# Kernel tuning notes

Measured on AMD Instinct MI355X. Metric: run time of the kernel, lower is better.

## Reference

```python
import jax, jax.numpy as jnp
import numpy as np

N_GENES = 15135
N_CMT = 1000
HID = 64


def _gcn_norm(edge_index, n):
    # add self-loops, compute symmetric normalization deg^-1/2 * deg^-1/2
    loop = jnp.arange(n, dtype=edge_index.dtype)
    src = jnp.concatenate([edge_index[0], loop])
    dst = jnp.concatenate([edge_index[1], loop])
    deg = jax.ops.segment_sum(jnp.ones_like(src, dtype=jnp.float32), dst, num_segments=n)
    dinv = jnp.where(deg > 0, 1.0 / jnp.sqrt(deg), 0.0)
    return src, dst, dinv[src] * dinv[dst]


def _gcn_conv(x, W, b, src, dst, norm, n):
    h = x @ W                                  # [bs, N, H]
    m = h[:, src, :] * norm[None, :, None]     # gather messages [bs, E, H]
    out = jnp.zeros_like(h).at[:, dst, :].add(m)
    return out + b


def setup_inputs():
    key = jax.random.key(0)
    ks = jax.random.split(key, 16)
    bs, nf, hfc, ncls, E, P = 8, 64, 128, 2, 242160, 120000
    s = 0.05
    return {
        "x": jax.random.normal(ks[0], (bs, N_GENES, nf), jnp.float32),
        "batch": jnp.zeros((bs,), jnp.int32),
        "edge_index": jax.random.randint(ks[1], (2, E), 0, N_GENES),
        "path_row": jax.random.randint(ks[2], (P,), 0, N_GENES),
        "path_col": jax.random.randint(ks[3], (P,), 0, N_CMT),
        "W1": jax.random.normal(ks[4], (nf, HID), jnp.float32) * s,
        "b1": jnp.zeros((HID,), jnp.float32),
        "W2": jax.random.normal(ks[5], (HID, HID), jnp.float32) * s,
        "b2": jnp.zeros((HID,), jnp.float32),
        "W3": jax.random.normal(ks[6], (HID, HID), jnp.float32) * s,
        "b3": jnp.zeros((HID,), jnp.float32),
        "fcW": jax.random.normal(ks[7], (3 * HID, 1), jnp.float32) * s,
        "fcb": jnp.zeros((1,), jnp.float32),
        "l1W": jax.random.normal(ks[8], (N_CMT, hfc), jnp.float32) * s,
        "l1b": jnp.zeros((hfc,), jnp.float32),
        "l2W": jax.random.normal(ks[9], (hfc, ncls), jnp.float32) * s,
        "l2b": jnp.zeros((ncls,), jnp.float32),
    }


def reference(x, batch, edge_index, path_row, path_col,
              W1, b1, W2, b2, W3, b3, fcW, fcb, l1W, l1b, l2W, l2b):
    bs, n = x.shape[0], x.shape[1]
    src, dst, norm = _gcn_norm(edge_index, n)

    x1 = jax.nn.relu(_gcn_conv(x, W1, b1, src, dst, norm, n))
    x2 = jax.nn.relu(_gcn_conv(x1, W2, b2, src, dst, norm, n))
    x3 = jax.nn.relu(_gcn_conv(x2, W3, b3, src, dst, norm, n))
    # mode='cat': torch.stack(xs, -1).view(bs, N, -1) -> layout [..., h*L + l]
    xc = jnp.stack([x1, x2, x3], axis=-1).reshape(bs, n, HID * 3)

    # pathway pooling: scatter_mean(x[row], col) over node axis
    xt = jnp.transpose(xc, (1, 0, 2))            # [N, bs, F]
    g = xt[path_row]                             # [P, bs, F]
    sums = jax.ops.segment_sum(g, path_col, num_segments=N_CMT)
    cnt = jax.ops.segment_sum(jnp.ones_like(path_col, dtype=xc.dtype), path_col, num_segments=N_CMT)
    pooled = sums / jnp.maximum(cnt, 1.0)[:, None, None]   # [n_cmt, bs, F]
    pooled = jnp.transpose(pooled, (1, 0, 2)).reshape(-1, HID * 3)  # [bs*n_cmt, F]

    h = (pooled @ fcW + fcb).reshape(bs, N_CMT)   # fc -> view(-1, n_cmt)
    h = jax.nn.relu(h @ l1W + l1b)                # (dropout is identity in eval)
    h = h @ l2W + l2b
    return jax.nn.log_softmax(h, axis=-1)
```

## Files before the change

kernel.cpp:

```cpp
#include <hip/hip_runtime.h>
#include <hip/hip_bf16.h>
#include <hip/hip_fp16.h>
#include <math.h>

#define HID 64

#if defined(__has_builtin)
#if __has_builtin(__builtin_amdgcn_cvt_pk_f32_fp8) && __has_builtin(__builtin_amdgcn_cvt_pk_fp8_f32)
#define HWFP8 1
#endif
#endif

typedef float vfloat2 __attribute__((ext_vector_type(2)));
typedef __attribute__((ext_vector_type(8))) short short8_t;
typedef __attribute__((ext_vector_type(4))) float f32x4;

union ABFrag { short8_t s; unsigned short u[8]; };


__device__ __forceinline__ unsigned short f2bf(float x) {
    unsigned int u = __float_as_uint(x);
    unsigned int r = u + 0x7fffu + ((u >> 16) & 1u);
    return (unsigned short)(r >> 16);
}

#ifndef HWFP8
__device__ __forceinline__ unsigned int enc8_sw(float a) {
    unsigned short hb = __half_as_ushort(__float2half(a));
    unsigned int r = (unsigned int)hb + 0x7fu + ((hb >> 8) & 1u);
    return (r >> 8) & 0xffu;
}
__device__ __forceinline__ float dec8_sw(unsigned int b) {
    return __half2float(__ushort_as_half((unsigned short)(b << 8)));
}
#endif

__device__ __forceinline__ unsigned int enc4(float a, float b, float c, float d) {
#ifdef HWFP8
    int r = __builtin_amdgcn_cvt_pk_fp8_f32(a, b, 0, false);
    r = __builtin_amdgcn_cvt_pk_fp8_f32(c, d, r, true);
    return (unsigned int)r;
#else
    return enc8_sw(a) | (enc8_sw(b) << 8) | (enc8_sw(c) << 16) | (enc8_sw(d) << 24);
#endif
}

__device__ __forceinline__ void dec4(unsigned int w, float* f) {
#ifdef HWFP8
    vfloat2 a = __builtin_amdgcn_cvt_pk_f32_fp8((int)w, false);
    vfloat2 b = __builtin_amdgcn_cvt_pk_f32_fp8((int)w, true);
    f[0] = a.x; f[1] = a.y; f[2] = b.x; f[3] = b.y;
#else
    f[0] = dec8_sw(w & 0xffu); f[1] = dec8_sw((w >> 8) & 0xffu);
    f[2] = dec8_sw((w >> 16) & 0xffu); f[3] = dec8_sw(w >> 24);
#endif
}

__device__ __forceinline__ void dec8(uint2 g, float* f) {
    dec4(g.x, f);
    dec4(g.y, f + 4);
}

__device__ __forceinline__ void gemm_epilogue(float* so, const f32x4* acc,
                                              unsigned int* Yq, float S,
                                              int r0w, int rowsTot, int lane) {
    int cc = lane & 15;
    int cr = (lane >> 4) * 4;
#pragma unroll
    for (int c = 0; c < 4; ++c) {
        so[(cr + 0) * 68 + c * 16 + cc] = acc[c][0];
        so[(cr + 1) * 68 + c * 16 + cc] = acc[c][1];
        so[(cr + 2) * 68 + c * 16 + cc] = acc[c][2];
        so[(cr + 3) * 68 + c * 16 + cc] = acc[c][3];
    }
    __syncthreads();
#pragma unroll
    for (int i = 0; i < 4; ++i) {
        int idx = lane + i * 64;
        int row = idx >> 4, ci = idx & 15;
        int grow = r0w + row;
        if (grow < rowsTot) {
            float4 v = *(const float4*)&so[row * 68 + ci * 4];
            Yq[(size_t)grow * 16 + ci] = enc4(v.x * S, v.y * S, v.z * S, v.w * S);
        }
    }
}

__global__ __launch_bounds__(256) void k_fused1(const float* __restrict__ x,
                                                const float* __restrict__ W1,
                                                unsigned int* __restrict__ Yq,
                                                float S, int N, int rowsTot, int gGf,
                                                const int* __restrict__ edst, int* __restrict__ deg, int E,
                                                const int* __restrict__ pcol, int* __restrict__ ccnt, int P,
                                                const float* __restrict__ W2, const float* __restrict__ W3,
                                                unsigned short* __restrict__ Wt) {
    __shared__ float sOut[4][16 * 68];
    __shared__ unsigned short sW[4096];
    int tid = threadIdx.x;
    if ((int)blockIdx.x < gGf) {
        int w = tid >> 6, lane = tid & 63;
        int cc = lane & 15, kg = (lane >> 4) * 8;
        float* so = &sOut[w][0];
#pragma unroll
        for (int i = 0; i < 16; ++i) {
            int idx = i * 256 + tid;
            int k = idx >> 6, c = idx & 63;
            sW[c * 64 + k] = f2bf(W1[idx]);
        }
        __syncthreads();
        ABFrag bf[2][4];
#pragma unroll
        for (int h = 0; h < 2; ++h)
#pragma unroll
            for (int c = 0; c < 4; ++c)
                bf[h][c].s = *(const short8_t*)&sW[(c * 16 + cc) * 64 + h * 32 + kg];

        int base = blockIdx.x * 128;
        ABFrag a[2];
        auto loadA = [&](int rA, ABFrag* dst) {
#pragma unroll
            for (int h = 0; h < 2; ++h) {
                if (rA < rowsTot) {
                    int n = rA >> 3, b = rA & 7;
                    const float* p = &x[((size_t)b * N + n) * 64 + h * 32 + kg];
                    float4 v0 = *(const float4*)p;
                    float4 v1 = *(const float4*)(p + 4);
                    dst[h].u[0] = f2bf(v0.x); dst[h].u[1] = f2bf(v0.y);
                    dst[h].u[2] = f2bf(v0.z); dst[h].u[3] = f2bf(v0.w);
                    dst[h].u[4] = f2bf(v1.x); dst[h].u[5] = f2bf(v1.y);
                    dst[h].u[6] = f2bf(v1.z); dst[h].u[7] = f2bf(v1.w);
                } else {
#pragma unroll
                    for (int j = 0; j < 8; ++j) dst[h].u[j] = 0;
                }
            }
        };
        loadA(base + w * 16 + (lane & 15), a);
#pragma unroll
        for (int t = 0; t < 2; ++t) {
            ABFrag an[2];
            if (t < 1) loadA(base + 64 + w * 16 + (lane & 15), an);
            f32x4 acc[4] = {f32x4{}, f32x4{}, f32x4{}, f32x4{}};
#pragma unroll
            for (int h = 0; h < 2; ++h)
#pragma unroll
                for (int c = 0; c < 4; ++c)
                    acc[c] = __builtin_amdgcn_mfma_f32_16x16x32_bf16(a[h].s, bf[h][c].s, acc[c], 0, 0, 0);
            gemm_epilogue(so, acc, Yq, S, base + t * 64 + w * 16, rowsTot, lane);
            if (t < 1) { a[0] = an[0]; a[1] = an[1]; __syncthreads(); }
        }
    } else {
        int cb = blockIdx.x - gGf;
        int nCB = gridDim.x - gGf;
        int gth = cb * 256 + tid;
        int GT = nCB * 256;
        for (int e = gth; e < E; e += GT) atomicAdd(&deg[edst[e]], 1);
        for (int p = gth; p < P; p += GT) atomicAdd(&ccnt[pcol[p]], 1);
        for (int i = gth; i < 2 * 4096; i += GT) {
            int l = i >> 12, r = i & 4095;
            int k = r >> 6, c = r & 63;
            const float* W = (l == 0) ? W2 : W3;
            Wt[(l << 12) + c * 64 + k] = f2bf(W[r]);
        }
    }
}


__global__ __launch_bounds__(256) void k_pre_scan(const int* __restrict__ deg, int* __restrict__ rowoff, int N,
                                                  const int* __restrict__ ccnt, int* __restrict__ coff, int NC,
                                                  float* __restrict__ dinv) {
    __shared__ int part[256];
    int t = threadIdx.x;
    int gth = blockIdx.x * blockDim.x + t;
    int GT = gridDim.x * blockDim.x;
    for (int i = gth; i < N; i += GT) dinv[i] = rsqrtf((float)(deg[i] + 1));

    const int* cnt = nullptr; int* off = nullptr; int n = 0;
    if (blockIdx.x == 0)      { cnt = deg;  off = rowoff; n = N; }
    else if (blockIdx.x == 1) { cnt = ccnt; off = coff;   n = NC; }
    else return;

    int CH = (n + 255) >> 8;
    int lo = min(t * CH, n), hi = min(lo + CH, n);
    int sum = 0;
    for (int i = lo; i < hi; ++i) sum += cnt[i];
    part[t] = sum;
    __syncthreads();
    for (int o = 1; o < 256; o <<= 1) {
        int v = (t >= o) ? part[t - o] : 0;
        __syncthreads();
        part[t] += v;
        __syncthreads();
    }
    int run = (t == 0) ? 0 : part[t - 1];
    for (int i = lo; i < hi; ++i) { off[i] = run; run += cnt[i]; }
    if (t == 255) off[n] = run;
}

__global__ __launch_bounds__(256) void k_pre_scatter(const int* __restrict__ esrc, const int* __restrict__ edst,
                                                     const float* __restrict__ dinv, const int* __restrict__ rowoff,
                                                     int* __restrict__ fill, int* __restrict__ ssrc,
                                                     float* __restrict__ snorm, int E,
                                                     const int* __restrict__ prow, const int* __restrict__ pcol,
                                                     const int* __restrict__ coff, int* __restrict__ cfill,
                                                     int* __restrict__ crow, int P) {
    int gth = blockIdx.x * blockDim.x + threadIdx.x;
    int GT = gridDim.x * blockDim.x;
    for (int e = gth; e < E; e += GT) {
        int s = esrc[e], d = edst[e];
        int pos = rowoff[d] + atomicAdd(&fill[d], 1);
        ssrc[pos]  = s;
        snorm[pos] = dinv[s] * dinv[d];
    }
    for (int p = gth; p < P; p += GT) {
        int c = pcol[p];
        int pos = coff[c] + atomicAdd(&cfill[c], 1);
        crow[pos] = prow[p];
    }
}


template<int LAYER>
__device__ __forceinline__ void agg_node(const uint2* __restrict__ Y,
                                         const int* __restrict__ rowoff,
                                         const int* __restrict__ ssrc,
                                         const float* __restrict__ snorm,
                                         const float* __restrict__ dinv,
                                         const float* bv, const float* wv,
                                         float* __restrict__ sArr,
                                         float invS, int n, int lane,
                                         float* accOut) {
    float dn = dinv[n];
    float w0 = dn * dn;
    float acc[8], f[8];
    dec8(Y[(size_t)n * 64 + lane], f);
#pragma unroll
    for (int k = 0; k < 8; ++k) acc[k] = w0 * f[k];

    int beg = rowoff[n], end = rowoff[n + 1];
    int i = beg;
    for (; i + 7 < end; i += 8) {
        int   sI[8];
        float wI[8];
        uint2 g[8];
#pragma unroll
        for (int u = 0; u < 8; ++u) { sI[u] = ssrc[i + u]; wI[u] = snorm[i + u]; }
#pragma unroll
        for (int u = 0; u < 8; ++u) g[u] = Y[(size_t)sI[u] * 64 + lane];
#pragma unroll
        for (int u = 0; u < 8; ++u) {
            dec8(g[u], f);
#pragma unroll
            for (int k = 0; k < 8; ++k) acc[k] = fmaf(wI[u], f[k], acc[k]);
        }
    }
    for (; i < end; ++i) {
        int s = ssrc[i];
        float w = snorm[i];
        dec8(Y[(size_t)s * 64 + lane], f);
#pragma unroll
        for (int k = 0; k < 8; ++k) acc[k] = fmaf(w, f[k], acc[k]);
    }

    float sv = 0.f;
#pragma unroll
    for (int k = 0; k < 8; ++k) {
        float o = fmaxf(fmaf(acc[k], invS, bv[k]), 0.f);
        accOut[k] = o;
        sv = fmaf(o, wv[k], sv);
    }
    sv += __shfl_down(sv, 4, 64);
    sv += __shfl_down(sv, 2, 64);
    sv += __shfl_down(sv, 1, 64);
    if ((lane & 7) == 0) {
        int b = lane >> 3;
        float* sp = sArr + (size_t)n * 8 + b;
        if (LAYER == 0) *sp = sv;
        else            *sp += sv;
    }
}

template<int LAYER>
__global__ __launch_bounds__(256) void k_aggemm(const uint2* __restrict__ Yin,
                                                const int* __restrict__ rowoff,
                                                const int* __restrict__ ssrc,
                                                const float* __restrict__ snorm,
                                                const float* __restrict__ dinv,
                                                const float* __restrict__ bias,
                                                const float* __restrict__ fcW,
                                                float* __restrict__ sArr, float invS,
                                                const unsigned short* __restrict__ Wt,
                                                unsigned int* __restrict__ Yout, float Sout,
                                                int N, int rowsTot) {
    __shared__ unsigned short sX[64 * 64];
    __shared__ float sOut[4][16 * 68];
    int tid = threadIdx.x;
    int w = tid >> 6, lane = tid & 63;
    int b = lane >> 3, hb = (lane & 7) * 8;

    float bv[8], wv[8];
#pragma unroll
    for (int k = 0; k < 8; ++k) { bv[k] = bias[hb + k]; wv[k] = fcW[3 * (hb + k) + LAYER]; }

    int n0 = blockIdx.x * 8;
#pragma unroll
    for (int j = 0; j < 2; ++j) {
        int ln = w * 2 + j;
        int n = n0 + ln;
        int r = ln * 8 + b;
        unsigned int byte = (unsigned int)(r * 128 + hb * 2) ^ ((unsigned int)(r & 7) << 4);
        short8_t* dst = (short8_t*)((char*)sX + byte);
        if (n < N) {
            float acc[8];
            agg_node<LAYER>(Yin, rowoff, ssrc, snorm, dinv, bv, wv, sArr, invS, n, lane, acc);
            ABFrag xr;
#pragma unroll
            for (int k = 0; k < 8; ++k) xr.u[k] = f2bf(acc[k]);
            *dst = xr.s;
        } else {
            ABFrag xr;
#pragma unroll
            for (int k = 0; k < 8; ++k) xr.u[k] = 0;
            *dst = xr.s;
        }
    }
    __syncthreads();

    int cc = lane & 15, kg = (lane >> 4) * 8;
    float* so = &sOut[w][0];
    ABFrag bf[2][4];
#pragma unroll
    for (int h = 0; h < 2; ++h)
#pragma unroll
        for (int c = 0; c < 4; ++c)
            bf[h][c].s = *(const short8_t*)&Wt[(size_t)(c * 16 + cc) * 64 + h * 32 + kg];

    int rA = w * 16 + (lane & 15);
    ABFrag a[2];
#pragma unroll
    for (int h = 0; h < 2; ++h) {
        unsigned int byte = (unsigned int)(rA * 128 + (h * 32 + kg) * 2) ^ ((unsigned int)(rA & 7) << 4);
        a[h].s = *(const short8_t*)((const char*)sX + byte);
    }
    f32x4 acc4[4] = {f32x4{}, f32x4{}, f32x4{}, f32x4{}};
#pragma unroll
    for (int h = 0; h < 2; ++h)
#pragma unroll
        for (int c = 0; c < 4; ++c)
            acc4[c] = __builtin_amdgcn_mfma_f32_16x16x32_bf16(a[h].s, bf[h][c].s, acc4[c], 0, 0, 0);
    gemm_epilogue(so, acc4, Yout, Sout, blockIdx.x * 64 + w * 16, rowsTot, lane);
}


template<int LAYER>
__global__ __launch_bounds__(256) void k_agg(const uint2* __restrict__ Y,
                                             const int* __restrict__ rowoff,
                                             const int* __restrict__ ssrc,
                                             const float* __restrict__ snorm,
                                             const float* __restrict__ dinv,
                                             const float* __restrict__ bias,
                                             const float* __restrict__ fcW,
                                             float* __restrict__ sArr,
                                             float invS, int N) {
    int n = blockIdx.x * 4 + (threadIdx.x >> 6);
    if (n >= N) return;
    int lane = threadIdx.x & 63;
    int hb = (lane & 7) * 8;
    float bv[8], wv[8];
#pragma unroll
    for (int k = 0; k < 8; ++k) { bv[k] = bias[hb + k]; wv[k] = fcW[3 * (hb + k) + LAYER]; }
    float acc[8];
    agg_node<LAYER>(Y, rowoff, ssrc, snorm, dinv, bv, wv, sArr, invS, n, lane, acc);
}


__global__ __launch_bounds__(128) void k_l1pool(const float* __restrict__ sArr,
                                                const int* __restrict__ coff,
                                                const int* __restrict__ crow,
                                                const float* __restrict__ fcb,
                                                const float* __restrict__ l1W,
                                                float* __restrict__ hpre,
                                                int* __restrict__ done,
                                                const float* __restrict__ l1b,
                                                const float* __restrict__ l2W,
                                                const float* __restrict__ l2b,
                                                float* __restrict__ out,
                                                int NC, int HFC, int bs, int NCLS,
                                                int CHUNK, int nBlocks) {
    __shared__ float hl[64];
    int b = blockIdx.y;
    int c0 = blockIdx.x * CHUNK;
    int j = threadIdx.x;
    int cend = min(c0 + CHUNK, NC);
    {
        int w = j >> 6, lane = j & 63, q = lane >> 4, s = lane & 15;
        float fcb0 = fcb[0];
        for (int c = c0 + w * 4 + q; c < cend; c += 8) {
            int beg = coff[c], end = coff[c + 1];
            float acc = 0.f;
            for (int i = beg + s; i < end; i += 16)
                acc += sArr[(size_t)crow[i] * 8 + b];
            acc += __shfl_down(acc, 8, 16);
            acc += __shfl_down(acc, 4, 16);
            acc += __shfl_down(acc, 2, 16);
            acc += __shfl_down(acc, 1, 16);
            if (s == 0)
                hl[c - c0] = acc / fmaxf((float)(end - beg), 1.f) + fcb0;
        }
    }
    __syncthreads();
    float acc = 0.f;
    for (int c = c0; c < cend; ++c) acc = fmaf(hl[c - c0], l1W[(size_t)c * HFC + j], acc);
    atomicAdd(&hpre[(size_t)b * HFC + j], acc);

    __threadfence();
    __syncthreads();
    __shared__ int amLast;
    if (j == 0) amLast = (atomicAdd(done, 1) == nBlocks - 1);
    __syncthreads();
    if (!amLast) return;
    __threadfence();

    __shared__ float sZ[64];
    int g = j >> 3, l8 = j & 7;
    int nout = bs * NCLS;
    float v = 0.f;
    int b2 = g / NCLS, k2 = g - b2 * NCLS;
    if (g < nout) {
        for (int jj = l8; jj < HFC; jj += 8) {
            float h = fmaxf(hpre[(size_t)b2 * HFC + jj] + l1b[jj], 0.f);
            v = fmaf(h, l2W[(size_t)jj * NCLS + k2], v);
        }
    }
    v += __shfl_down(v, 4, 8);
    v += __shfl_down(v, 2, 8);
    v += __shfl_down(v, 1, 8);
    if (l8 == 0 && g < nout) sZ[g] = v + l2b[k2];
    __syncthreads();
    if (j < bs) {
        float m = -1e30f;
        for (int c = 0; c < NCLS; ++c) m = fmaxf(m, sZ[j * NCLS + c]);
        float s = 0.f;
        for (int c = 0; c < NCLS; ++c) s += expf(sZ[j * NCLS + c] - m);
        float lse = m + logf(s);
        for (int c = 0; c < NCLS; ++c) out[j * NCLS + c] = sZ[j * NCLS + c] - lse;
    }
}


extern "C" void kernel_launch(void* const* d_in, const int* in_sizes, int n_in,
                              void* d_out, int out_size, void* d_ws, size_t ws_size,
                              hipStream_t stream) {
    const float* x   = (const float*)d_in[0];
    const int* eidx  = (const int*)d_in[2];
    const int* prow  = (const int*)d_in[3];
    const int* pcol  = (const int*)d_in[4];
    const float* W1  = (const float*)d_in[5];
    const float* b1  = (const float*)d_in[6];
    const float* W2  = (const float*)d_in[7];
    const float* b2  = (const float*)d_in[8];
    const float* W3  = (const float*)d_in[9];
    const float* b3  = (const float*)d_in[10];
    const float* fcW = (const float*)d_in[11];
    const float* fcb = (const float*)d_in[12];
    const float* l1W = (const float*)d_in[13];
    const float* l1b = (const float*)d_in[14];
    const float* l2W = (const float*)d_in[15];
    const float* l2b = (const float*)d_in[16];
    float* out = (float*)d_out;

    const int bs   = in_sizes[1];
    const int E    = in_sizes[2] / 2;
    const int P    = in_sizes[3];
    const int N    = in_sizes[0] / (bs * HID);
    const int HFC  = in_sizes[14];
    const int NC   = in_sizes[13] / HFC;
    const int NCLS = in_sizes[15] / HFC;
    const int rows = N * bs;

    const int* esrc = eidx;
    const int* edst = eidx + E;

    size_t off = 0;
    auto alloc = [&](size_t bytes) -> void* {
        void* r = (char*)d_ws + off;
        off += (bytes + 255) & ~(size_t)255;
        return r;
    };
    char* zbase   = (char*)d_ws;
    int*   deg    = (int*)  alloc((size_t)N * 4);
    int*   fill   = (int*)  alloc((size_t)N * 4);
    int*   ccnt   = (int*)  alloc((size_t)NC * 4);
    int*   cfill  = (int*)  alloc((size_t)NC * 4);
    float* hpre   = (float*)alloc((size_t)bs * HFC * 4);
    int*   done   = (int*)  alloc(4);
    size_t zspan  = off;
    float* dinv   = (float*)alloc((size_t)N * 4);
    int*   rowoff = (int*)  alloc(((size_t)N + 1) * 4);
    int*   coff   = (int*)  alloc(((size_t)NC + 1) * 4);
    int*   crow   = (int*)  alloc((size_t)P * 4);
    int*   ssrc   = (int*)  alloc((size_t)E * 4);
    float* snorm  = (float*)alloc((size_t)E * 4);
    unsigned int* Yqa  = (unsigned int*)alloc((size_t)rows * HID);
    unsigned int* Yqb  = (unsigned int*)alloc((size_t)rows * HID);
    float* sArr   = (float*)alloc((size_t)rows * 4);
    unsigned short* Wt = (unsigned short*)alloc((size_t)2 * 64 * 64 * 2);

    hipMemsetAsync(zbase, 0, zspan, stream);

    const float S1 = 1.f,  iS1 = 1.f;
    const float S2 = 16.f, iS2 = 1.f / 16.f;
    const float S3 = 128.f, iS3 = 1.f / 128.f;

    int gG2 = (rows + 127) / 128;
    int gF  = (N + 7) / 8;
    int gA  = (N + 3) / 4;
    int gPre = 512;

    k_fused1<<<gG2 + gPre, 256, 0, stream>>>(x, W1, Yqa, S1, N, rows, gG2,
                                             edst, deg, E, pcol, ccnt, P, W2, W3, Wt);
    k_pre_scan<<<64, 256, 0, stream>>>(deg, rowoff, N, ccnt, coff, NC, dinv);
    k_pre_scatter<<<gPre, 256, 0, stream>>>(esrc, edst, dinv, rowoff, fill, ssrc, snorm, E,
                                            prow, pcol, coff, cfill, crow, P);

    k_aggemm<0><<<gF, 256, 0, stream>>>((const uint2*)Yqa, rowoff, ssrc, snorm, dinv, b1, fcW,
                                        sArr, iS1, Wt, Yqb, S2, N, rows);
    k_aggemm<1><<<gF, 256, 0, stream>>>((const uint2*)Yqb, rowoff, ssrc, snorm, dinv, b2, fcW,
                                        sArr, iS2, Wt + 4096, Yqa, S3, N, rows);
    k_agg<2><<<gA, 256, 0, stream>>>((const uint2*)Yqa, rowoff, ssrc, snorm, dinv, b3, fcW,
                                     sArr, iS3, N);

    const int CHUNK = 40;
    dim3 gL1((NC + CHUNK - 1) / CHUNK, bs);
    int nBlocks = gL1.x * gL1.y;
    k_l1pool<<<gL1, 128, 0, stream>>>(sArr, coff, crow, fcb, l1W, hpre, done,
                                      l1b, l2W, l2b, out, NC, HFC, bs, NCLS, CHUNK, nBlocks);
}
```

Before: 350.4 us.

## Pad neighbor gather into 8-wide batches and alias LDS buffers in fused agg-GEMM

The aggregation loop now handles the remainder edges with masked 8-wide batches (zero weight, clamped index) instead of a serial scalar tail, and defers the self-loop decode until after the first batch of gathers is issued so more loads are in flight. The fused aggregation+GEMM kernel also unions the sX staging buffer with the sOut epilogue buffer, shrinking LDS per block to raise occupancy, at the cost of an extra __syncthreads before the epilogue. Masked lanes issue redundant loads, and the extra barrier adds a sync point.

```diff
diff --git a/kernel.cpp b/kernel.cpp
--- a/kernel.cpp
+++ b/kernel.cpp
@@ -219,7 +219,6 @@
     }
 }
 
-
 template<int LAYER>
 __device__ __forceinline__ void agg_node(const uint2* __restrict__ Y,
                                          const int* __restrict__ rowoff,
@@ -232,21 +231,32 @@
                                          float* accOut) {
     float dn = dinv[n];
     float w0 = dn * dn;
-    float acc[8], f[8];
-    dec8(Y[(size_t)n * 64 + lane], f);
-#pragma unroll
-    for (int k = 0; k < 8; ++k) acc[k] = w0 * f[k];
-
     int beg = rowoff[n], end = rowoff[n + 1];
-    int i = beg;
-    for (; i + 7 < end; i += 8) {
+
+    uint2 gs = Y[(size_t)n * 64 + lane];
+    float acc[8] = {0.f, 0.f, 0.f, 0.f, 0.f, 0.f, 0.f, 0.f};
+    float f[8];
+    bool haveSelf = false;
+
+    for (int i = beg; i < end; i += 8) {
         int   sI[8];
         float wI[8];
         uint2 g[8];
 #pragma unroll
-        for (int u = 0; u < 8; ++u) { sI[u] = ssrc[i + u]; wI[u] = snorm[i + u]; }
+        for (int u = 0; u < 8; ++u) {
+            int valid = (i + u < end);
+            int idx = valid ? (i + u) : i;
+            sI[u] = ssrc[idx];
+            wI[u] = valid ? snorm[idx] : 0.f;
+        }
 #pragma unroll
         for (int u = 0; u < 8; ++u) g[u] = Y[(size_t)sI[u] * 64 + lane];
+        if (!haveSelf) {
+            dec8(gs, f);
+#pragma unroll
+            for (int k = 0; k < 8; ++k) acc[k] = w0 * f[k];
+            haveSelf = true;
+        }
 #pragma unroll
         for (int u = 0; u < 8; ++u) {
             dec8(g[u], f);
@@ -254,12 +264,10 @@
             for (int k = 0; k < 8; ++k) acc[k] = fmaf(wI[u], f[k], acc[k]);
         }
     }
-    for (; i < end; ++i) {
-        int s = ssrc[i];
-        float w = snorm[i];
-        dec8(Y[(size_t)s * 64 + lane], f);
-#pragma unroll
-        for (int k = 0; k < 8; ++k) acc[k] = fmaf(w, f[k], acc[k]);
+    if (!haveSelf) {
+        dec8(gs, f);
+#pragma unroll
+        for (int k = 0; k < 8; ++k) acc[k] = w0 * f[k];
     }
 
     float sv = 0.f;
@@ -292,8 +300,8 @@
                                                 const unsigned short* __restrict__ Wt,
                                                 unsigned int* __restrict__ Yout, float Sout,
                                                 int N, int rowsTot) {
-    __shared__ unsigned short sX[64 * 64];
-    __shared__ float sOut[4][16 * 68];
+    struct ShU { union { unsigned short sX[64 * 64]; float sOut[4][16 * 68]; }; };
+    __shared__ ShU sh;
     int tid = threadIdx.x;
     int w = tid >> 6, lane = tid & 63;
     int b = lane >> 3, hb = (lane & 7) * 8;
@@ -309,7 +317,7 @@
         int n = n0 + ln;
         int r = ln * 8 + b;
         unsigned int byte = (unsigned int)(r * 128 + hb * 2) ^ ((unsigned int)(r & 7) << 4);
-        short8_t* dst = (short8_t*)((char*)sX + byte);
+        short8_t* dst = (short8_t*)((char*)sh.sX + byte);
         if (n < N) {
             float acc[8];
             agg_node<LAYER>(Yin, rowoff, ssrc, snorm, dinv, bv, wv, sArr, invS, n, lane, acc);
@@ -327,7 +335,6 @@
     __syncthreads();
 
     int cc = lane & 15, kg = (lane >> 4) * 8;
-    float* so = &sOut[w][0];
     ABFrag bf[2][4];
 #pragma unroll
     for (int h = 0; h < 2; ++h)
@@ -340,7 +347,7 @@
 #pragma unroll
     for (int h = 0; h < 2; ++h) {
         unsigned int byte = (unsigned int)(rA * 128 + (h * 32 + kg) * 2) ^ ((unsigned int)(rA & 7) << 4);
-        a[h].s = *(const short8_t*)((const char*)sX + byte);
+        a[h].s = *(const short8_t*)((const char*)sh.sX + byte);
     }
     f32x4 acc4[4] = {f32x4{}, f32x4{}, f32x4{}, f32x4{}};
 #pragma unroll
@@ -348,7 +355,8 @@
 #pragma unroll
         for (int c = 0; c < 4; ++c)
             acc4[c] = __builtin_amdgcn_mfma_f32_16x16x32_bf16(a[h].s, bf[h][c].s, acc4[c], 0, 0, 0);
-    gemm_epilogue(so, acc4, Yout, Sout, blockIdx.x * 64 + w * 16, rowsTot, lane);
+    __syncthreads();
+    gemm_epilogue(&sh.sOut[w][0], acc4, Yout, Sout, blockIdx.x * 64 + w * 16, rowsTot, lane);
 }
 
 
```

New measurement: 341.9 us. 1.03x faster.
